# Kernel tuning notes

Hardware: AMD Instinct MI355X
Metric: run time of the kernel (lower is better)

## Reference

```python
import jax, jax.numpy as jnp
import numpy as np

N = 16777216  # number of samples
G = 16        # number of distinct group ids


def setup_inputs() -> dict:
    key = jax.random.key(0)
    k1, k2, k3, k4, k5 = jax.random.split(key, 5)
    u1 = jax.random.uniform(k1, (N,), dtype=jnp.float32)
    u2 = jax.random.uniform(k2, (N,), dtype=jnp.float32)
    u3 = jax.random.uniform(k3, (N,), dtype=jnp.float32)
    u4 = jax.random.uniform(k4, (N,), dtype=jnp.float32)
    return {
        "shape": 0.5 + 1.0 * u1,              # Weibull shape b in [0.5, 1.5]
        "scale": 0.8 + 1.2 * u2,              # Weibull scale a in [0.8, 2.0]
        "time": 0.1 + 2.9 * u3,               # survival time y in [0.1, 3.0]
        "event": (u4 > 0.5).astype(jnp.float32),  # event indicator u in {0,1}
        "lengths": jnp.arange(N, dtype=jnp.int32),   # only len(lengths)=N is used
        "group": jax.random.randint(k5, (N,), 0, G, dtype=jnp.int32),
    }


def reference(shape, scale, time, event, lengths, group):
    b, a, y, u = shape, scale, time, event
    # Per-sample Weibull NLL (torch.mean over a scalar is identity).
    hazard0 = (y + 1e-35 / a) ** b
    hazard1 = (y + 1.0 / a) ** b
    per_sample = -(u * jnp.log(jnp.exp(hazard1 - hazard0) - 1.0) - hazard1)  # [N]
    # Overall loss: sum / len(lengths) == mean over samples.
    loss = jnp.mean(per_sample)
    # Per-group mean via segment-sum (dict accumulation in the original).
    ones = jnp.ones_like(per_sample)
    counts = jax.ops.segment_sum(ones, group, num_segments=G)         # [G]
    gsum = jax.ops.segment_sum(per_sample, group, num_segments=G)     # [G]
    group_losses = gsum / jnp.maximum(counts, 1.0)                    # [G]
    return loss, group_losses
```

## Files before the change

### kernel.cpp

```cpp
#include <hip/hip_runtime.h>


namespace {
constexpr int NG = 16;
constexpr int BLOCK = 256;
constexpr float LOG2E = 1.4426950408889634f;
constexpr float LN2   = 0.6931471805599453f;
}

__device__ __forceinline__ float flog2(float x) { return __builtin_amdgcn_logf(x); }
__device__ __forceinline__ float fexp2(float x) { return __builtin_amdgcn_exp2f(x); }
__device__ __forceinline__ float frcp(float x)  { return __builtin_amdgcn_rcpf(x); }

__device__ __forceinline__ float per_sample(float b, float a, float y, float u) {
    const float inva = frcp(a);
    const float h1 = fexp2(b * flog2(y + inva));
    const float h0 = fexp2(b * flog2(y));
    const float em1 = fexp2((h1 - h0) * LOG2E) - 1.0f;
    const float t = flog2(em1) * LN2;
    return __builtin_fmaf(-u, t, h1);
}

__global__ __launch_bounds__(BLOCK) void gssl_main_kernel(
    const float* __restrict__ bptr,
    const float* __restrict__ aptr,
    const float* __restrict__ yptr,
    const float* __restrict__ uptr,
    const int*   __restrict__ gptr,
    float* __restrict__ ws,
    int n4, int n)
{
    __shared__ float sbin[2 * NG];
    const int tid = threadIdx.x;
    if (tid < 2 * NG) sbin[tid] = 0.0f;
    __syncthreads();

    float asum[NG], acnt[NG];
    #pragma unroll
    for (int q = 0; q < NG; ++q) { asum[q] = 0.0f; acnt[q] = 0.0f; }

    const int stride = gridDim.x * BLOCK;
    for (int i = blockIdx.x * BLOCK + tid; i < n4; i += stride) {
        const float4 b4 = reinterpret_cast<const float4*>(bptr)[i];
        const float4 a4 = reinterpret_cast<const float4*>(aptr)[i];
        const float4 y4 = reinterpret_cast<const float4*>(yptr)[i];
        const float4 u4 = reinterpret_cast<const float4*>(uptr)[i];
        const int4   g4 = reinterpret_cast<const int4*>(gptr)[i];
        const float bb[4] = {b4.x, b4.y, b4.z, b4.w};
        const float aa[4] = {a4.x, a4.y, a4.z, a4.w};
        const float yy[4] = {y4.x, y4.y, y4.z, y4.w};
        const float uu[4] = {u4.x, u4.y, u4.z, u4.w};
        const int   gg[4] = {g4.x, g4.y, g4.z, g4.w};
        #pragma unroll
        for (int k = 0; k < 4; ++k) {
            const float ps = per_sample(bb[k], aa[k], yy[k], uu[k]);
            const int g = gg[k];
            #pragma unroll
            for (int q = 0; q < NG; ++q) {
                const float m = (g == q) ? 1.0f : 0.0f;
                asum[q] = __builtin_fmaf(m, ps, asum[q]);
                acnt[q] += m;
            }
        }
    }

    #pragma unroll
    for (int q = 0; q < NG; ++q) {
        #pragma unroll
        for (int off = 32; off > 0; off >>= 1) {
            asum[q] += __shfl_xor(asum[q], off, 64);
            acnt[q] += __shfl_xor(acnt[q], off, 64);
        }
    }

    if ((tid & 63) == 0) {
        #pragma unroll
        for (int q = 0; q < NG; ++q) {
            atomicAdd(&sbin[q], asum[q]);
            atomicAdd(&sbin[NG + q], acnt[q]);
        }
    }
    __syncthreads();

    if (tid < 2 * NG) atomicAdd(&ws[tid], sbin[tid]);

    if (blockIdx.x == 0 && tid == 0) {
        for (int i = n4 * 4; i < n; ++i) {
            const float ps = per_sample(bptr[i], aptr[i], yptr[i], uptr[i]);
            atomicAdd(&ws[gptr[i]], ps);
            atomicAdd(&ws[NG + gptr[i]], 1.0f);
        }
    }
}

__global__ __launch_bounds__(64) void gssl_final_kernel(
    const float* __restrict__ ws, float* __restrict__ out, float invN)
{
    const int t = threadIdx.x;
    if (t < NG) {
        const float gs = ws[t];
        const float gc = ws[NG + t];
        out[1 + t] = gs / fmaxf(gc, 1.0f);
    }
    float v = (t < NG) ? ws[t] : 0.0f;
    #pragma unroll
    for (int off = 32; off > 0; off >>= 1) v += __shfl_down(v, off);
    if (t == 0) out[0] = v * invN;
}

extern "C" void kernel_launch(void* const* d_in, const int* in_sizes, int n_in,
                              void* d_out, int out_size, void* d_ws, size_t ws_size,
                              hipStream_t stream) {
    const float* shape_p = (const float*)d_in[0];
    const float* scale_p = (const float*)d_in[1];
    const float* time_p  = (const float*)d_in[2];
    const float* event_p = (const float*)d_in[3];
    const int*   group_p = (const int*)d_in[5];
    float* out = (float*)d_out;
    float* ws  = (float*)d_ws;

    const int n  = in_sizes[0];
    const int n4 = n >> 2;

    hipMemsetAsync(ws, 0, 2 * NG * sizeof(float), stream);

    int blocks = 2048;
    const int need = (n4 + BLOCK - 1) / BLOCK;
    if (need < blocks) blocks = (need > 0) ? need : 1;

    hipLaunchKernelGGL(gssl_main_kernel, dim3(blocks), dim3(BLOCK), 0, stream,
                       shape_p, scale_p, time_p, event_p, group_p, ws, n4, n);
    hipLaunchKernelGGL(gssl_final_kernel, dim3(1), dim3(64), 0, stream,
                       ws, out, 1.0f / (float)n);
}
```

Measured before the change: 80.50 us.

## Use contiguous per-block chunks, 2x unrolled loads, and ballot-based group counts

Each block now processes one contiguous chunk of float4 elements instead of a grid-stride range, and the loop is unrolled two-wide so more loads are in flight at once. Per-group counts are taken with a wave ballot plus popcount into integer accumulators, which removes 16 count shuffle reductions at the end. The ballot is still issued per group per element inside the hot loop, so it adds scalar work there and may cost about as much as the per-lane adds it replaces.

Measured after the change: 84.61 us. 1.05x slower.

```diff
diff --git a/kernel.cpp b/kernel.cpp
--- a/kernel.cpp
+++ b/kernel.cpp
@@ -28,19 +28,23 @@
     const float* __restrict__ uptr,
     const int*   __restrict__ gptr,
     float* __restrict__ ws,
-    int n4, int n)
+    int per_block, int n4, int n)
 {
     __shared__ float sbin[2 * NG];
     const int tid = threadIdx.x;
     if (tid < 2 * NG) sbin[tid] = 0.0f;
     __syncthreads();
 
-    float asum[NG], acnt[NG];
+    float asum[NG];
+    int   acnt[NG];
     #pragma unroll
-    for (int q = 0; q < NG; ++q) { asum[q] = 0.0f; acnt[q] = 0.0f; }
+    for (int q = 0; q < NG; ++q) { asum[q] = 0.0f; acnt[q] = 0; }
 
-    const int stride = gridDim.x * BLOCK;
-    for (int i = blockIdx.x * BLOCK + tid; i < n4; i += stride) {
+    const int base = blockIdx.x * per_block;
+    const int rem  = n4 - base;
+    const int jend = (rem < per_block) ? (rem < 0 ? 0 : rem) : per_block;
+
+    auto do4 = [&](int i) {
         const float4 b4 = reinterpret_cast<const float4*>(bptr)[i];
         const float4 a4 = reinterpret_cast<const float4*>(aptr)[i];
         const float4 y4 = reinterpret_cast<const float4*>(yptr)[i];
@@ -57,27 +61,32 @@
             const int g = gg[k];
             #pragma unroll
             for (int q = 0; q < NG; ++q) {
-                const float m = (g == q) ? 1.0f : 0.0f;
-                asum[q] = __builtin_fmaf(m, ps, asum[q]);
-                acnt[q] += m;
+                const bool eq = (g == q);
+                asum[q] += eq ? ps : 0.0f;
+                acnt[q] += (int)__popcll(__ballot(eq));
             }
         }
+    };
+
+    int j = tid;
+    for (; j + BLOCK < jend; j += 2 * BLOCK) {
+        do4(base + j);
+        do4(base + j + BLOCK);
     }
+    if (j < jend) do4(base + j);
 
     #pragma unroll
     for (int q = 0; q < NG; ++q) {
         #pragma unroll
-        for (int off = 32; off > 0; off >>= 1) {
+        for (int off = 32; off > 0; off >>= 1)
             asum[q] += __shfl_xor(asum[q], off, 64);
-            acnt[q] += __shfl_xor(acnt[q], off, 64);
-        }
     }
 
     if ((tid & 63) == 0) {
         #pragma unroll
         for (int q = 0; q < NG; ++q) {
             atomicAdd(&sbin[q], asum[q]);
-            atomicAdd(&sbin[NG + q], acnt[q]);
+            atomicAdd(&sbin[NG + q], (float)acnt[q]);
         }
     }
     __syncthreads();
@@ -124,12 +133,12 @@
 
     hipMemsetAsync(ws, 0, 2 * NG * sizeof(float), stream);
 
-    int blocks = 2048;
-    const int need = (n4 + BLOCK - 1) / BLOCK;
-    if (need < blocks) blocks = (need > 0) ? need : 1;
+    const int blocks = 2048;
+    const int per_block = (n4 + blocks - 1) / blocks;
 
     hipLaunchKernelGGL(gssl_main_kernel, dim3(blocks), dim3(BLOCK), 0, stream,
-                       shape_p, scale_p, time_p, event_p, group_p, ws, n4, n);
+                       shape_p, scale_p, time_p, event_p, group_p, ws,
+                       per_block, n4, n);
     hipLaunchKernelGGL(gssl_final_kernel, dim3(1), dim3(64), 0, stream,
                        ws, out, 1.0f / (float)n);
 }
```
